# Kernel tuning notes

Measured on AMD Instinct MI355X. Metric: run time of the kernel, lower is better.

The kernel has to match this reference:

```python
import jax, jax.numpy as jnp
import numpy as np

N_MLP = 1024  # number of independent tiny MLPs
D_IN, D_HID, D_OUT = 2, 4, 1
B = 16384


def setup_inputs() -> dict:
    key = jax.random.key(0)
    k = jax.random.split(key, 6)
    x = jax.random.normal(k[0], (B, N_MLP), dtype=jnp.float32)
    x_aug = jax.random.normal(k[1], (B, N_MLP), dtype=jnp.float32)
    # Stacked per-MLP parameters (nn.Linear default init ~ U(-1/sqrt(fan_in), 1/sqrt(fan_in)))
    s1 = 1.0 / np.sqrt(D_IN)
    s2 = 1.0 / np.sqrt(D_HID)
    W1 = jax.random.uniform(k[2], (N_MLP, D_HID, D_IN), jnp.float32, -s1, s1)
    b1 = jax.random.uniform(k[3], (N_MLP, D_HID), jnp.float32, -s1, s1)
    W2 = jax.random.uniform(k[4], (N_MLP, D_OUT, D_HID), jnp.float32, -s2, s2)
    b2 = jax.random.uniform(k[5], (N_MLP, D_OUT), jnp.float32, -s2, s2)
    return {"x": x, "x_aug": x_aug, "W1": W1, "b1": b1, "W2": W2, "b2": b2}


def reference(x, x_aug, W1, b1, W2, b2):
    # data: [B, N, 2] — pair (original, augmented) per feature
    data = jnp.stack([x, x_aug], axis=-1)
    # batched tiny GEMM across the N_MLP axis: [B,N,2] x [N,4,2] -> [B,N,4]
    h = jax.nn.relu(jnp.einsum('bne,nhe->bnh', data, W1) + b1)
    # [B,N,4] x [N,1,4] -> [B,N,1]
    o = jnp.einsum('bnh,noh->bno', h, W2) + b2
    # concat over dim1 of per-MLP [B,1] outputs == squeeze -> [B,N]; mean over N -> [B]
    return jnp.mean(o[..., 0], axis=1)
```

## Files before the change

kernel.cpp:

```cpp
#include <hip/hip_runtime.h>


constexpr int N_MLP = 1024;
constexpr int BATCH = 16384;
constexpr int ROWS = 16;
constexpr int NTHREADS = 256;

__global__ __launch_bounds__(NTHREADS)
void disc_mlp_kernel(const float* __restrict__ x,
                     const float* __restrict__ xa,
                     const float* __restrict__ W1,
                     const float* __restrict__ b1,
                     const float* __restrict__ W2,
                     const float* __restrict__ b2,
                     float* __restrict__ out)
{
    const int t  = threadIdx.x;
    const int b0 = blockIdx.x * ROWS;
    const int n0 = t * 4;

    float A[4][4];
    float C[4][4];
    float B1[4][4];
    float V[4][4];
    float b2sum = 0.0f;
    {
        const float4* w1v = reinterpret_cast<const float4*>(W1) + (size_t)n0 * 2;
        const float4* b1v = reinterpret_cast<const float4*>(b1) + n0;
        const float4* w2v = reinterpret_cast<const float4*>(W2) + n0;
#pragma unroll
        for (int nn = 0; nn < 4; ++nn) {
            float4 p0 = w1v[nn * 2];
            float4 p1 = w1v[nn * 2 + 1];
            A[nn][0] = p0.x; C[nn][0] = p0.y;
            A[nn][1] = p0.z; C[nn][1] = p0.w;
            A[nn][2] = p1.x; C[nn][2] = p1.y;
            A[nn][3] = p1.z; C[nn][3] = p1.w;
            float4 bb = b1v[nn];
            B1[nn][0] = bb.x; B1[nn][1] = bb.y; B1[nn][2] = bb.z; B1[nn][3] = bb.w;
            float4 ww = w2v[nn];
            V[nn][0] = ww.x; V[nn][1] = ww.y; V[nn][2] = ww.z; V[nn][3] = ww.w;
            b2sum += b2[n0 + nn];
        }
    }

    float acc[ROWS];
#pragma unroll
    for (int r = 0; r < ROWS; ++r) acc[r] = 0.0f;

    const size_t rowbase = (size_t)b0 * N_MLP + n0;
#pragma unroll 4
    for (int r = 0; r < ROWS; ++r) {
        const float4 xv  = *reinterpret_cast<const float4*>(x  + rowbase + (size_t)r * N_MLP);
        const float4 xav = *reinterpret_cast<const float4*>(xa + rowbase + (size_t)r * N_MLP);
        const float xe[4]  = {xv.x,  xv.y,  xv.z,  xv.w};
        const float xae[4] = {xav.x, xav.y, xav.z, xav.w};
        float s = b2sum;
#pragma unroll
        for (int nn = 0; nn < 4; ++nn) {
#pragma unroll
            for (int j = 0; j < 4; ++j) {
                float h = fmaf(A[nn][j], xe[nn], fmaf(C[nn][j], xae[nn], B1[nn][j]));
                h = fmaxf(h, 0.0f);
                s = fmaf(V[nn][j], h, s);
            }
        }
        acc[r] = s;
    }

    __shared__ float lds[NTHREADS / 64][ROWS];
    const int lane = t & 63;
    const int wave = t >> 6;
#pragma unroll
    for (int r = 0; r < ROWS; ++r) {
        float v = acc[r];
        v += __shfl_down(v, 32);
        v += __shfl_down(v, 16);
        v += __shfl_down(v, 8);
        v += __shfl_down(v, 4);
        v += __shfl_down(v, 2);
        v += __shfl_down(v, 1);
        if (lane == 0) lds[wave][r] = v;
    }
    __syncthreads();
    if (t < ROWS) {
        float s = lds[0][t] + lds[1][t] + lds[2][t] + lds[3][t];
        out[b0 + t] = s * (1.0f / (float)N_MLP);
    }
}

extern "C" void kernel_launch(void* const* d_in, const int* in_sizes, int n_in,
                              void* d_out, int out_size, void* d_ws, size_t ws_size,
                              hipStream_t stream) {
    const float* x  = (const float*)d_in[0];
    const float* xa = (const float*)d_in[1];
    const float* W1 = (const float*)d_in[2];
    const float* b1 = (const float*)d_in[3];
    const float* W2 = (const float*)d_in[4];
    const float* b2 = (const float*)d_in[5];
    float* out = (float*)d_out;

    disc_mlp_kernel<<<BATCH / ROWS, NTHREADS, 0, stream>>>(x, xa, W1, b1, W2, b2, out);
}
```

Measured before the change: 158.7 us.

## Split MLP axis across blocks and combine partial means with atomics

Each block now covers a quarter of the MLP axis for 16 rows, with one MLP per thread. Loads become coalesced scalar loads issued in batches of eight rows. Partial row sums are accumulated into the output with atomicAdd after a separate zeroing kernel. The aim is more blocks and more memory-level parallelism for a bandwidth-bound stream. The cost is an extra kernel launch, atomic contention, and nondeterministic summation order.

New measurement: 150.9 us. 1.05x faster.

```diff
diff --git a/kernel.cpp b/kernel.cpp
--- a/kernel.cpp
+++ b/kernel.cpp
@@ -4,7 +4,14 @@
 constexpr int N_MLP = 1024;
 constexpr int BATCH = 16384;
 constexpr int ROWS = 16;
+constexpr int CH = 8;
 constexpr int NTHREADS = 256;
+constexpr int NQ = N_MLP / NTHREADS;
+
+__global__ __launch_bounds__(256)
+void zero_out_kernel(float* __restrict__ out) {
+    out[blockIdx.x * 256 + threadIdx.x] = 0.0f;
+}
 
 __global__ __launch_bounds__(NTHREADS)
 void disc_mlp_kernel(const float* __restrict__ x,
@@ -16,56 +23,49 @@
                      float* __restrict__ out)
 {
     const int t  = threadIdx.x;
-    const int b0 = blockIdx.x * ROWS;
-    const int n0 = t * 4;
+    const int q  = blockIdx.x & (NQ - 1);
+    const int rb = blockIdx.x >> 2;
+    const int b0 = rb * ROWS;
+    const int n  = q * NTHREADS + t;
 
-    float A[4][4];
-    float C[4][4];
-    float B1[4][4];
-    float V[4][4];
-    float b2sum = 0.0f;
+    float A[4], C[4], B1r[4], V[4], b2r;
     {
-        const float4* w1v = reinterpret_cast<const float4*>(W1) + (size_t)n0 * 2;
-        const float4* b1v = reinterpret_cast<const float4*>(b1) + n0;
-        const float4* w2v = reinterpret_cast<const float4*>(W2) + n0;
-#pragma unroll
-        for (int nn = 0; nn < 4; ++nn) {
-            float4 p0 = w1v[nn * 2];
-            float4 p1 = w1v[nn * 2 + 1];
-            A[nn][0] = p0.x; C[nn][0] = p0.y;
-            A[nn][1] = p0.z; C[nn][1] = p0.w;
-            A[nn][2] = p1.x; C[nn][2] = p1.y;
-            A[nn][3] = p1.z; C[nn][3] = p1.w;
-            float4 bb = b1v[nn];
-            B1[nn][0] = bb.x; B1[nn][1] = bb.y; B1[nn][2] = bb.z; B1[nn][3] = bb.w;
-            float4 ww = w2v[nn];
-            V[nn][0] = ww.x; V[nn][1] = ww.y; V[nn][2] = ww.z; V[nn][3] = ww.w;
-            b2sum += b2[n0 + nn];
-        }
+        const float4* w1v = reinterpret_cast<const float4*>(W1) + (size_t)n * 2;
+        float4 p0 = w1v[0];
+        float4 p1 = w1v[1];
+        A[0] = p0.x; C[0] = p0.y;
+        A[1] = p0.z; C[1] = p0.w;
+        A[2] = p1.x; C[2] = p1.y;
+        A[3] = p1.z; C[3] = p1.w;
+        float4 bb = reinterpret_cast<const float4*>(b1)[n];
+        B1r[0] = bb.x; B1r[1] = bb.y; B1r[2] = bb.z; B1r[3] = bb.w;
+        float4 ww = reinterpret_cast<const float4*>(W2)[n];
+        V[0] = ww.x; V[1] = ww.y; V[2] = ww.z; V[3] = ww.w;
+        b2r = b2[n];
     }
 
     float acc[ROWS];
+    const size_t base = (size_t)b0 * N_MLP + n;
+
 #pragma unroll
-    for (int r = 0; r < ROWS; ++r) acc[r] = 0.0f;
-
-    const size_t rowbase = (size_t)b0 * N_MLP + n0;
-#pragma unroll 4
-    for (int r = 0; r < ROWS; ++r) {
-        const float4 xv  = *reinterpret_cast<const float4*>(x  + rowbase + (size_t)r * N_MLP);
-        const float4 xav = *reinterpret_cast<const float4*>(xa + rowbase + (size_t)r * N_MLP);
-        const float xe[4]  = {xv.x,  xv.y,  xv.z,  xv.w};
-        const float xae[4] = {xav.x, xav.y, xav.z, xav.w};
-        float s = b2sum;
+    for (int rc = 0; rc < ROWS; rc += CH) {
+        float xe[CH], xae[CH];
 #pragma unroll
-        for (int nn = 0; nn < 4; ++nn) {
+        for (int i = 0; i < CH; ++i) {
+            xe[i]  = x [base + (size_t)(rc + i) * N_MLP];
+            xae[i] = xa[base + (size_t)(rc + i) * N_MLP];
+        }
+#pragma unroll
+        for (int i = 0; i < CH; ++i) {
+            float s = b2r;
 #pragma unroll
             for (int j = 0; j < 4; ++j) {
-                float h = fmaf(A[nn][j], xe[nn], fmaf(C[nn][j], xae[nn], B1[nn][j]));
+                float h = fmaf(A[j], xe[i], fmaf(C[j], xae[i], B1r[j]));
                 h = fmaxf(h, 0.0f);
-                s = fmaf(V[nn][j], h, s);
+                s = fmaf(V[j], h, s);
             }
+            acc[rc + i] = s;
         }
-        acc[r] = s;
     }
 
     __shared__ float lds[NTHREADS / 64][ROWS];
@@ -84,8 +84,8 @@
     }
     __syncthreads();
     if (t < ROWS) {
-        float s = lds[0][t] + lds[1][t] + lds[2][t] + lds[3][t];
-        out[b0 + t] = s * (1.0f / (float)N_MLP);
+        float s = (lds[0][t] + lds[1][t]) + (lds[2][t] + lds[3][t]);
+        atomicAdd(out + b0 + t, s * (1.0f / (float)N_MLP));
     }
 }
 
@@ -100,5 +100,6 @@
     const float* b2 = (const float*)d_in[5];
     float* out = (float*)d_out;
 
-    disc_mlp_kernel<<<BATCH / ROWS, NTHREADS, 0, stream>>>(x, xa, W1, b1, W2, b2, out);
+    zero_out_kernel<<<BATCH / 256, 256, 0, stream>>>(out);
+    disc_mlp_kernel<<<(BATCH / ROWS) * NQ, NTHREADS, 0, stream>>>(x, xa, W1, b1, W2, b2, out);
 }
```

## Split MLP eval into per-wave partial kernel plus separate row reduction kernel

Applied to the files above, without the earlier changes.

The single fused kernel is replaced by two launches. The first assigns each wave an 8-row by 256-MLP segment, issues all x/x_aug loads up front before the weight loads, and writes per-lane partial sums to the workspace without any shuffle or LDS reduction. A second kernel reduces the 256 partials per row into the mean. This removes in-kernel shuffle trees and block syncs and raises memory-level parallelism, at the cost of an extra launch and a 16 MB workspace write and read.

New measurement: 166.4 us. 1.05x slower.

```diff
diff --git a/kernel.cpp b/kernel.cpp
--- a/kernel.cpp
+++ b/kernel.cpp
@@ -3,90 +3,89 @@
 
 constexpr int N_MLP = 1024;
 constexpr int BATCH = 16384;
-constexpr int ROWS = 16;
+constexpr int RPW = 8;
+constexpr int NSEG = 4;
 constexpr int NTHREADS = 256;
 
-__global__ __launch_bounds__(NTHREADS)
-void disc_mlp_kernel(const float* __restrict__ x,
-                     const float* __restrict__ xa,
-                     const float* __restrict__ W1,
-                     const float* __restrict__ b1,
-                     const float* __restrict__ W2,
-                     const float* __restrict__ b2,
-                     float* __restrict__ out)
+__global__ __launch_bounds__(NTHREADS, 1)
+void mlp_partial_kernel(const float* __restrict__ x,
+                        const float* __restrict__ xa,
+                        const float* __restrict__ W1,
+                        const float* __restrict__ b1,
+                        const float* __restrict__ W2,
+                        const float* __restrict__ b2,
+                        float* __restrict__ partial)
 {
-    const int t  = threadIdx.x;
-    const int b0 = blockIdx.x * ROWS;
-    const int n0 = t * 4;
+    const int l   = threadIdx.x & 63;
+    const int w   = threadIdx.x >> 6;
+    const int wu  = blockIdx.x * 4 + w;
+    const int seg = wu & (NSEG - 1);
+    const int oct = wu >> 2;
+    const int b0  = oct * RPW;
+    const int n0  = seg * 256 + l * 4;
 
-    float A[4][4];
-    float C[4][4];
-    float B1[4][4];
-    float V[4][4];
-    float b2sum = 0.0f;
-    {
-        const float4* w1v = reinterpret_cast<const float4*>(W1) + (size_t)n0 * 2;
-        const float4* b1v = reinterpret_cast<const float4*>(b1) + n0;
-        const float4* w2v = reinterpret_cast<const float4*>(W2) + n0;
+    const size_t pbase = (size_t)b0 * N_MLP + n0;
+    float4 xr[RPW], ar[RPW];
 #pragma unroll
-        for (int nn = 0; nn < 4; ++nn) {
-            float4 p0 = w1v[nn * 2];
-            float4 p1 = w1v[nn * 2 + 1];
-            A[nn][0] = p0.x; C[nn][0] = p0.y;
-            A[nn][1] = p0.z; C[nn][1] = p0.w;
-            A[nn][2] = p1.x; C[nn][2] = p1.y;
-            A[nn][3] = p1.z; C[nn][3] = p1.w;
-            float4 bb = b1v[nn];
-            B1[nn][0] = bb.x; B1[nn][1] = bb.y; B1[nn][2] = bb.z; B1[nn][3] = bb.w;
-            float4 ww = w2v[nn];
-            V[nn][0] = ww.x; V[nn][1] = ww.y; V[nn][2] = ww.z; V[nn][3] = ww.w;
-            b2sum += b2[n0 + nn];
+    for (int r = 0; r < RPW; ++r) {
+        xr[r] = *reinterpret_cast<const float4*>(x  + pbase + (size_t)r * N_MLP);
+        ar[r] = *reinterpret_cast<const float4*>(xa + pbase + (size_t)r * N_MLP);
+    }
+    const float4* w1v = reinterpret_cast<const float4*>(W1) + (size_t)n0 * 2;
+    const float4* b1v = reinterpret_cast<const float4*>(b1) + n0;
+    const float4* w2v = reinterpret_cast<const float4*>(W2) + n0;
+    float4 p[8], bbv[4], wwv[4];
+#pragma unroll
+    for (int i = 0; i < 8; ++i) p[i] = w1v[i];
+#pragma unroll
+    for (int m = 0; m < 4; ++m) { bbv[m] = b1v[m]; wwv[m] = w2v[m]; }
+    const float4 b2q = reinterpret_cast<const float4*>(b2)[n0 / 4];
+    const float b2sum = (b2q.x + b2q.y) + (b2q.z + b2q.w);
+
+    float s[RPW];
+#pragma unroll
+    for (int r = 0; r < RPW; ++r) {
+        const float xe[4]  = {xr[r].x, xr[r].y, xr[r].z, xr[r].w};
+        const float xae[4] = {ar[r].x, ar[r].y, ar[r].z, ar[r].w};
+        float acc = b2sum;
+#pragma unroll
+        for (int m = 0; m < 4; ++m) {
+            const float A0 = p[2*m].x,   C0 = p[2*m].y;
+            const float A1 = p[2*m].z,   C1 = p[2*m].w;
+            const float A2 = p[2*m+1].x, C2 = p[2*m+1].y;
+            const float A3 = p[2*m+1].z, C3 = p[2*m+1].w;
+            float h0 = fmaxf(fmaf(A0, xe[m], fmaf(C0, xae[m], bbv[m].x)), 0.0f);
+            float h1 = fmaxf(fmaf(A1, xe[m], fmaf(C1, xae[m], bbv[m].y)), 0.0f);
+            float h2 = fmaxf(fmaf(A2, xe[m], fmaf(C2, xae[m], bbv[m].z)), 0.0f);
+            float h3 = fmaxf(fmaf(A3, xe[m], fmaf(C3, xae[m], bbv[m].w)), 0.0f);
+            acc = fmaf(wwv[m].x, h0, acc);
+            acc = fmaf(wwv[m].y, h1, acc);
+            acc = fmaf(wwv[m].z, h2, acc);
+            acc = fmaf(wwv[m].w, h3, acc);
         }
+        s[r] = acc;
     }
 
-    float acc[ROWS];
+    float* pb = partial + (size_t)b0 * 256 + seg * 64 + l;
 #pragma unroll
-    for (int r = 0; r < ROWS; ++r) acc[r] = 0.0f;
+    for (int r = 0; r < RPW; ++r) pb[(size_t)r * 256] = s[r];
+}
 
-    const size_t rowbase = (size_t)b0 * N_MLP + n0;
-#pragma unroll 4
-    for (int r = 0; r < ROWS; ++r) {
-        const float4 xv  = *reinterpret_cast<const float4*>(x  + rowbase + (size_t)r * N_MLP);
-        const float4 xav = *reinterpret_cast<const float4*>(xa + rowbase + (size_t)r * N_MLP);
-        const float xe[4]  = {xv.x,  xv.y,  xv.z,  xv.w};
-        const float xae[4] = {xav.x, xav.y, xav.z, xav.w};
-        float s = b2sum;
-#pragma unroll
-        for (int nn = 0; nn < 4; ++nn) {
-#pragma unroll
-            for (int j = 0; j < 4; ++j) {
-                float h = fmaf(A[nn][j], xe[nn], fmaf(C[nn][j], xae[nn], B1[nn][j]));
-                h = fmaxf(h, 0.0f);
-                s = fmaf(V[nn][j], h, s);
-            }
-        }
-        acc[r] = s;
-    }
-
-    __shared__ float lds[NTHREADS / 64][ROWS];
-    const int lane = t & 63;
-    const int wave = t >> 6;
-#pragma unroll
-    for (int r = 0; r < ROWS; ++r) {
-        float v = acc[r];
-        v += __shfl_down(v, 32);
-        v += __shfl_down(v, 16);
-        v += __shfl_down(v, 8);
-        v += __shfl_down(v, 4);
-        v += __shfl_down(v, 2);
-        v += __shfl_down(v, 1);
-        if (lane == 0) lds[wave][r] = v;
-    }
-    __syncthreads();
-    if (t < ROWS) {
-        float s = lds[0][t] + lds[1][t] + lds[2][t] + lds[3][t];
-        out[b0 + t] = s * (1.0f / (float)N_MLP);
-    }
+__global__ __launch_bounds__(NTHREADS)
+void reduce_kernel(const float* __restrict__ partial, float* __restrict__ out)
+{
+    const int l = threadIdx.x & 63;
+    const int w = threadIdx.x >> 6;
+    const int b = blockIdx.x * 4 + w;
+    const float4 v = reinterpret_cast<const float4*>(partial + (size_t)b * 256)[l];
+    float s = (v.x + v.y) + (v.z + v.w);
+    s += __shfl_down(s, 32);
+    s += __shfl_down(s, 16);
+    s += __shfl_down(s, 8);
+    s += __shfl_down(s, 4);
+    s += __shfl_down(s, 2);
+    s += __shfl_down(s, 1);
+    if (l == 0) out[b] = s * (1.0f / (float)N_MLP);
 }
 
 extern "C" void kernel_launch(void* const* d_in, const int* in_sizes, int n_in,
@@ -98,7 +97,10 @@
     const float* b1 = (const float*)d_in[3];
     const float* W2 = (const float*)d_in[4];
     const float* b2 = (const float*)d_in[5];
-    float* out = (float*)d_out;
+    float* out     = (float*)d_out;
+    float* partial = (float*)d_ws;
 
-    disc_mlp_kernel<<<BATCH / ROWS, NTHREADS, 0, stream>>>(x, xa, W1, b1, W2, b2, out);
+    mlp_partial_kernel<<<(BATCH / RPW) * NSEG / 4, NTHREADS, 0, stream>>>(
+        x, xa, W1, b1, W2, b2, partial);
+    reduce_kernel<<<BATCH / 4, NTHREADS, 0, stream>>>(partial, out);
 }
```
